# Kernel tuning notes

Hardware: AMD Instinct MI355X
Metric: run time of the kernel (lower is better)

Reference implementation:

```python
import jax, jax.numpy as jnp
import numpy as np

HEAD_COUNT = 6  # module scales by head_count**-0.5, not head_size
SCALE = HEAD_COUNT ** (-0.5)


def setup_inputs() -> dict:
    key = jax.random.key(0)
    kx, kq, kk, kv = jax.random.split(key, 4)
    B, T, C, H = 512, 128, 384, 64
    x = jax.random.normal(kx, (B, T, C), dtype=jnp.float32)
    init = (1.0 / np.sqrt(C)).astype(np.float32)
    Wq = jax.random.normal(kq, (C, H), dtype=jnp.float32) * init
    Wk = jax.random.normal(kk, (C, H), dtype=jnp.float32) * init
    Wv = jax.random.normal(kv, (C, H), dtype=jnp.float32) * init
    return {"x": x, "Wq": Wq, "Wk": Wk, "Wv": Wv}


def reference(x, Wq, Wk, Wv):
    # x: [B, T, C]; Wq/Wk/Wv: [C, H]
    q = jnp.einsum('btc,ch->bth', x, Wq)
    k = jnp.einsum('btc,ch->bth', x, Wk)
    v = jnp.einsum('btc,ch->bth', x, Wv)
    # scores: [B, T, T], scaled by head_count**-0.5 (faithful to source)
    scores = jnp.einsum('bth,bsh->bts', q, k) * SCALE
    T = x.shape[1]
    causal = jnp.tril(jnp.ones((T, T), dtype=bool))
    scores = jnp.where(causal, scores, -jnp.inf)
    weights = jax.nn.softmax(scores, axis=-1)
    # dropout omitted (eval mode / identity for reference baseline)
    return jnp.einsum('bts,bsh->bth', weights, v)
```

## Files before the change

kernel.cpp:

```cpp
#include <hip/hip_runtime.h>
#include <hip/hip_bf16.h>


#define B_ 512
#define T_ 128
#define C_ 384
#define H_ 64

typedef __bf16 bf16;
typedef __attribute__((ext_vector_type(8))) __bf16 bf16x8;
typedef __attribute__((ext_vector_type(4))) __bf16 bf16x4;
typedef __attribute__((ext_vector_type(4))) float f32x4;


__launch_bounds__(256, 2)
__global__ void head_fused(const float* __restrict__ x,
                           const float* __restrict__ Wq,
                           const float* __restrict__ Wk,
                           const float* __restrict__ Wv,
                           float* __restrict__ out)
{
    __shared__ bf16 lds[32256];
    bf16* Ws  = lds;
    bf16* Qs  = lds + 7680;
    bf16* Ks  = lds + 15872;
    bf16* Vts = lds + 24064;
    bf16* Ps  = lds + 7680;

    const int tid  = threadIdx.x;
    const int w    = tid >> 6;
    const int lane = tid & 63;
    const int lm   = lane & 15;
    const int quad = lane >> 4;
    const int b    = blockIdx.x;

    const float* xb = x + (size_t)b * (T_ * C_);

    f32x4 acc[2][12];
#pragma unroll
    for (int i = 0; i < 2; ++i)
#pragma unroll
        for (int t = 0; t < 12; ++t) acc[i][t] = (f32x4){0.f, 0.f, 0.f, 0.f};

    for (int kc = 0; kc < 12; ++kc) {
#pragma unroll
        for (int it = 0; it < 6; ++it) {
            int u   = tid + it * 256;
            int h   = u & 63;
            int rem = u >> 6;
            int j   = rem >> 3;
            int k4  = rem & 7;
            const float* Wp = (j == 0) ? Wq : (j == 1) ? Wk : Wv;
            const float* g  = Wp + (kc * 32 + k4 * 4) * H_ + h;
            float f0 = g[0], f1 = g[64], f2 = g[128], f3 = g[192];
            bf16x4 v4 = {(bf16)f0, (bf16)f1, (bf16)f2, (bf16)f3};
            *(bf16x4*)&Ws[(j * 64 + h) * 40 + k4 * 4] = v4;
        }
        __syncthreads();

        bf16x8 afr[2];
#pragma unroll
        for (int i = 0; i < 2; ++i) {
            const float4* xp =
                (const float4*)(xb + (32 * w + 16 * i + lm) * C_ + kc * 32 + quad * 8);
            float4 p0 = xp[0], p1 = xp[1];
            afr[i] = (bf16x8){(bf16)p0.x, (bf16)p0.y, (bf16)p0.z, (bf16)p0.w,
                              (bf16)p1.x, (bf16)p1.y, (bf16)p1.z, (bf16)p1.w};
        }
#pragma unroll
        for (int tn = 0; tn < 12; ++tn) {
            bf16x8 bfr = *(const bf16x8*)&Ws[(16 * tn + lm) * 40 + quad * 8];
            acc[0][tn] = __builtin_amdgcn_mfma_f32_16x16x32_bf16(afr[0], bfr, acc[0][tn], 0, 0, 0);
            acc[1][tn] = __builtin_amdgcn_mfma_f32_16x16x32_bf16(afr[1], bfr, acc[1][tn], 0, 0, 0);
        }
        __syncthreads();
    }

#pragma unroll
    for (int i = 0; i < 2; ++i) {
#pragma unroll
        for (int tn = 0; tn < 12; ++tn) {
            int gn = 16 * tn + lm;
            int j = gn >> 6, h = gn & 63;
            int m0 = 32 * w + 16 * i + quad * 4;
            if (j == 2) {
                bf16x4 v4 = {(bf16)acc[i][tn][0], (bf16)acc[i][tn][1],
                             (bf16)acc[i][tn][2], (bf16)acc[i][tn][3]};
                int pc = (m0 & 7) | ((((m0 >> 3) ^ (h & 15)) & 15) << 3);
                *(bf16x4*)&Vts[h * 128 + pc] = v4;
            } else {
                bf16* dst = (j == 0) ? Qs : Ks;
#pragma unroll
                for (int r = 0; r < 4; ++r) {
                    int m = m0 + r;
                    int pc = (h & 7) | ((((h >> 3) ^ (m & 7)) & 7) << 3);
                    dst[m * 64 + pc] = (bf16)acc[i][tn][r];
                }
            }
        }
    }
    __syncthreads();

    const float SCALE = 0.40824829046386307f;
    const int tmg0 = w, tmg1 = 7 - w;

    f32x4 sacc[2][8];
#pragma unroll
    for (int i = 0; i < 2; ++i)
#pragma unroll
        for (int t = 0; t < 8; ++t) sacc[i][t] = (f32x4){0.f, 0.f, 0.f, 0.f};

#pragma unroll
    for (int i = 0; i < 2; ++i) {
        const int tm = i ? tmg1 : tmg0;
        const int mrow = 16 * tm + lm;
        bf16x8 qa[2];
#pragma unroll
        for (int ks = 0; ks < 2; ++ks) {
            int phys = ((ks * 4 + quad) ^ (mrow & 7)) & 7;
            qa[ks] = *(const bf16x8*)&Qs[mrow * 64 + phys * 8];
        }
#pragma unroll
        for (int tn = 0; tn < 8; ++tn) {
            if (tn <= tm) {
                int nrow = 16 * tn + lm;
#pragma unroll
                for (int ks = 0; ks < 2; ++ks) {
                    int phys = ((ks * 4 + quad) ^ (nrow & 7)) & 7;
                    bf16x8 kb = *(const bf16x8*)&Ks[nrow * 64 + phys * 8];
                    sacc[i][tn] =
                        __builtin_amdgcn_mfma_f32_16x16x32_bf16(qa[ks], kb, sacc[i][tn], 0, 0, 0);
                }
            }
        }
    }

#pragma unroll
    for (int i = 0; i < 2; ++i) {
        const int tm = i ? tmg1 : tmg0;
#pragma unroll
        for (int r = 0; r < 4; ++r) {
            int m = 16 * tm + quad * 4 + r;
            float mx = -1e30f;
#pragma unroll
            for (int tn = 0; tn < 8; ++tn) {
                if (tn <= tm) {
                    int n = 16 * tn + lm;
                    float v = (n <= m) ? sacc[i][tn][r] * SCALE : -1e30f;
                    sacc[i][tn][r] = v;
                    mx = fmaxf(mx, v);
                }
            }
#pragma unroll
            for (int off = 1; off < 16; off <<= 1) mx = fmaxf(mx, __shfl_xor(mx, off, 16));
            float sum = 0.f;
#pragma unroll
            for (int tn = 0; tn < 8; ++tn) {
                if (tn <= tm) {
                    float e = __expf(sacc[i][tn][r] - mx);
                    sacc[i][tn][r] = e;
                    sum += e;
                }
            }
#pragma unroll
            for (int off = 1; off < 16; off <<= 1) sum += __shfl_xor(sum, off, 16);
            float inv = 1.f / sum;
#pragma unroll
            for (int tn = 0; tn < 8; ++tn) {
                if (tn <= tm) sacc[i][tn][r] *= inv;
            }
        }
    }

    __syncthreads();

#pragma unroll
    for (int i = 0; i < 2; ++i) {
        const int tm = i ? tmg1 : tmg0;
#pragma unroll
        for (int tn = 0; tn < 8; ++tn) {
            if (tn <= tm) {
                int n = 16 * tn + lm;
#pragma unroll
                for (int r = 0; r < 4; ++r) {
                    int m = 16 * tm + quad * 4 + r;
                    int pc = (n & 7) | ((((n >> 3) ^ (m & 15)) & 15) << 3);
                    Ps[m * 128 + pc] = (bf16)sacc[i][tn][r];
                }
            }
        }
        if ((tm & 1) == 0) {
            int m = 16 * tm + lm;
            int c0 = 16 * (tm + 1) + quad * 4;
            int pc = (c0 & 7) | ((((c0 >> 3) ^ (m & 15)) & 15) << 3);
            *(bf16x4*)&Ps[m * 128 + pc] =
                (bf16x4){(bf16)0.f, (bf16)0.f, (bf16)0.f, (bf16)0.f};
        }
    }

    f32x4 oacc[2][4];
#pragma unroll
    for (int i = 0; i < 2; ++i)
#pragma unroll
        for (int t = 0; t < 4; ++t) oacc[i][t] = (f32x4){0.f, 0.f, 0.f, 0.f};

#pragma unroll
    for (int i = 0; i < 2; ++i) {
        const int tm = i ? tmg1 : tmg0;
        const int mrow = 16 * tm + lm;
        const int nks = (tm + 2) >> 1;
        for (int ks = 0; ks < nks; ++ks) {
            int unit = ks * 4 + quad;
            int phys = (unit ^ (mrow & 15)) & 15;
            bf16x8 pa = *(const bf16x8*)&Ps[mrow * 128 + phys * 8];
#pragma unroll
            for (int th = 0; th < 4; ++th) {
                int hrow = 16 * th + lm;
                int ph2 = (unit ^ (hrow & 15)) & 15;
                bf16x8 vb = *(const bf16x8*)&Vts[hrow * 128 + ph2 * 8];
                oacc[i][th] =
                    __builtin_amdgcn_mfma_f32_16x16x32_bf16(pa, vb, oacc[i][th], 0, 0, 0);
            }
        }
    }

    float* ob = out + (size_t)b * (T_ * H_);
#pragma unroll
    for (int i = 0; i < 2; ++i) {
        const int tm = i ? tmg1 : tmg0;
#pragma unroll
        for (int th = 0; th < 4; ++th) {
            int h = 16 * th + lm;
#pragma unroll
            for (int r = 0; r < 4; ++r) {
                int m = 16 * tm + quad * 4 + r;
                ob[m * 64 + h] = oacc[i][th][r];
            }
        }
    }
}

extern "C" void kernel_launch(void* const* d_in, const int* in_sizes, int n_in,
                              void* d_out, int out_size, void* d_ws, size_t ws_size,
                              hipStream_t stream) {
    const float* x  = (const float*)d_in[0];
    const float* Wq = (const float*)d_in[1];
    const float* Wk = (const float*)d_in[2];
    const float* Wv = (const float*)d_in[3];
    float* o = (float*)d_out;
    head_fused<<<dim3(B_), dim3(256), 0, stream>>>(x, Wq, Wk, Wv, o);
}
```

Before: 172.6 us.

## Prepack weights into MFMA fragment layout and double-buffer x loads

A small pre-kernel converts Wq/Wk/Wv to bf16 once per call and lays them out in the per-lane MFMA B-fragment order in the workspace. The main kernel then reads the B fragments straight from global memory (L2-resident) instead of having every block re-convert and stage the weights through LDS with two barriers per k-chunk. The x loads for the projection are software-pipelined across two register buffers. LDS footprint shrinks, which may help occupancy. The cost is an extra kernel launch and per-MFMA global loads for the weights.

```diff
diff --git a/kernel.cpp b/kernel.cpp
--- a/kernel.cpp
+++ b/kernel.cpp
@@ -12,20 +12,36 @@
 typedef __attribute__((ext_vector_type(4))) __bf16 bf16x4;
 typedef __attribute__((ext_vector_type(4))) float f32x4;
 
+__global__ void build_wt(const float* __restrict__ Wq, const float* __restrict__ Wk,
+                         const float* __restrict__ Wv, bf16* __restrict__ Wt)
+{
+    int t = blockIdx.x * 256 + threadIdx.x;
+    if (t >= 12 * 12 * 64) return;
+    int lane = t & 63;
+    int tn   = (t >> 6) % 12;
+    int kc   = t / (12 * 64);
+    int lm = lane & 15, quad = lane >> 4;
+    int n = tn * 16 + lm;
+    int j = n >> 6, h = n & 63;
+    const float* Wp = (j == 0) ? Wq : (j == 1) ? Wk : Wv;
+    int k0 = kc * 32 + quad * 8;
+    bf16x8 v;
+#pragma unroll
+    for (int e = 0; e < 8; ++e) v[e] = (bf16)Wp[(k0 + e) * H_ + h];
+    *(bf16x8*)&Wt[t * 8] = v;
+}
+
 
 __launch_bounds__(256, 2)
 __global__ void head_fused(const float* __restrict__ x,
-                           const float* __restrict__ Wq,
-                           const float* __restrict__ Wk,
-                           const float* __restrict__ Wv,
+                           const bf16* __restrict__ Wt,
                            float* __restrict__ out)
 {
-    __shared__ bf16 lds[32256];
-    bf16* Ws  = lds;
-    bf16* Qs  = lds + 7680;
-    bf16* Ks  = lds + 15872;
-    bf16* Vts = lds + 24064;
-    bf16* Ps  = lds + 7680;
+    __shared__ bf16 lds[24576];
+    bf16* Qs  = lds;
+    bf16* Ks  = lds + 8192;
+    bf16* Vts = lds + 16384;
+    bf16* Ps  = lds;
 
     const int tid  = threadIdx.x;
     const int w    = tid >> 6;
@@ -42,38 +58,39 @@
 #pragma unroll
         for (int t = 0; t < 12; ++t) acc[i][t] = (f32x4){0.f, 0.f, 0.f, 0.f};
 
-    for (int kc = 0; kc < 12; ++kc) {
-#pragma unroll
-        for (int it = 0; it < 6; ++it) {
-            int u   = tid + it * 256;
-            int h   = u & 63;
-            int rem = u >> 6;
-            int j   = rem >> 3;
-            int k4  = rem & 7;
-            const float* Wp = (j == 0) ? Wq : (j == 1) ? Wk : Wv;
-            const float* g  = Wp + (kc * 32 + k4 * 4) * H_ + h;
-            float f0 = g[0], f1 = g[64], f2 = g[128], f3 = g[192];
-            bf16x4 v4 = {(bf16)f0, (bf16)f1, (bf16)f2, (bf16)f3};
-            *(bf16x4*)&Ws[(j * 64 + h) * 40 + k4 * 4] = v4;
-        }
-        __syncthreads();
-
-        bf16x8 afr[2];
-#pragma unroll
-        for (int i = 0; i < 2; ++i) {
-            const float4* xp =
-                (const float4*)(xb + (32 * w + 16 * i + lm) * C_ + kc * 32 + quad * 8);
-            float4 p0 = xp[0], p1 = xp[1];
-            afr[i] = (bf16x8){(bf16)p0.x, (bf16)p0.y, (bf16)p0.z, (bf16)p0.w,
-                              (bf16)p1.x, (bf16)p1.y, (bf16)p1.z, (bf16)p1.w};
-        }
+    const float* xr0 = xb + (32 * w + lm) * C_ + quad * 8;
+    const float* xr1 = xb + (32 * w + 16 + lm) * C_ + quad * 8;
+    const bf16*  wl  = Wt + lane * 8;
+
+    float4 xA[4], xB[4];
+
+    auto LD = [&](int kc, float4* xr) {
+        xr[0] = *(const float4*)(xr0 + kc * 32);
+        xr[1] = *(const float4*)(xr0 + kc * 32 + 4);
+        xr[2] = *(const float4*)(xr1 + kc * 32);
+        xr[3] = *(const float4*)(xr1 + kc * 32 + 4);
+    };
+    auto CHUNK = [&](int kc, const float4* xr) {
+        bf16x8 a0 = {(bf16)xr[0].x, (bf16)xr[0].y, (bf16)xr[0].z, (bf16)xr[0].w,
+                     (bf16)xr[1].x, (bf16)xr[1].y, (bf16)xr[1].z, (bf16)xr[1].w};
+        bf16x8 a1 = {(bf16)xr[2].x, (bf16)xr[2].y, (bf16)xr[2].z, (bf16)xr[2].w,
+                     (bf16)xr[3].x, (bf16)xr[3].y, (bf16)xr[3].z, (bf16)xr[3].w};
+        const bf16* wp = wl + kc * 6144;
 #pragma unroll
         for (int tn = 0; tn < 12; ++tn) {
-            bf16x8 bfr = *(const bf16x8*)&Ws[(16 * tn + lm) * 40 + quad * 8];
-            acc[0][tn] = __builtin_amdgcn_mfma_f32_16x16x32_bf16(afr[0], bfr, acc[0][tn], 0, 0, 0);
-            acc[1][tn] = __builtin_amdgcn_mfma_f32_16x16x32_bf16(afr[1], bfr, acc[1][tn], 0, 0, 0);
-        }
-        __syncthreads();
+            bf16x8 bfr = *(const bf16x8*)(wp + tn * 512);
+            acc[0][tn] = __builtin_amdgcn_mfma_f32_16x16x32_bf16(a0, bfr, acc[0][tn], 0, 0, 0);
+            acc[1][tn] = __builtin_amdgcn_mfma_f32_16x16x32_bf16(a1, bfr, acc[1][tn], 0, 0, 0);
+        }
+    };
+
+    LD(0, xA);
+#pragma unroll
+    for (int kc = 0; kc < 12; kc += 2) {
+        LD(kc + 1, xB);
+        CHUNK(kc, xA);
+        if (kc + 2 < 12) LD(kc + 2, xA);
+        CHUNK(kc + 1, xB);
     }
 
 #pragma unroll
@@ -248,5 +265,7 @@
     const float* Wk = (const float*)d_in[2];
     const float* Wv = (const float*)d_in[3];
     float* o = (float*)d_out;
-    head_fused<<<dim3(B_), dim3(256), 0, stream>>>(x, Wq, Wk, Wv, o);
+    bf16* Wt = (bf16*)d_ws;
+    build_wt<<<dim3(36), dim3(256), 0, stream>>>(Wq, Wk, Wv, Wt);
+    head_fused<<<dim3(B_), dim3(256), 0, stream>>>(x, Wt, o);
 }
```

New measurement: 185.8 us. +7.6%, slower.
